# Optimization experiments

Measured on AMD Instinct MI355X. Metric: run time of the kernel, lower is better.

Reference implementation:

```python
import jax, jax.numpy as jnp
import numpy as np

EPS = 1e-6

def _rmsnorm(x, w):
    # fp32 RMSNorm over last dim
    var = jnp.mean(x * x, axis=-1, keepdims=True)
    return w * (x * jax.lax.rsqrt(var + EPS))

def setup_inputs() -> dict:
    key = jax.random.key(0)
    ks = jax.random.split(key, 6)
    S, D, H = 4096, 1024, 16
    HD = D // H
    return {
        "hidden_states": jax.random.normal(ks[0], (S, D), jnp.float32),
        "qkv_w": jax.random.normal(ks[1], (3 * D, D), jnp.float32) * 0.02,
        "qkv_b": jnp.zeros((3 * D,), jnp.float32),
        "proj_w": jax.random.normal(ks[2], (D, D), jnp.float32) * 0.02,
        "proj_b": jnp.zeros((D,), jnp.float32),
        "q_norm_w": jnp.ones((D,), jnp.float32),
        "k_norm_w": jnp.ones((D,), jnp.float32),
        "rotary_freqs": jax.random.normal(ks[3], (S, HD // 2), jnp.float32),
        "cu_seqlens": jnp.array([0, 1024, 2048, 3072, 4096], jnp.int32),
        "num_heads": 16,
    }

def reference(hidden_states, qkv_w, qkv_b, proj_w, proj_b, q_norm_w, k_norm_w, rotary_freqs, cu_seqlens, num_heads):
    S, D = hidden_states.shape
    H = num_heads
    hd = D // H
    # QKV projection
    qkv = hidden_states @ qkv_w.T + qkv_b           # [S, 3D]
    qkv = qkv.reshape(S, 3, H, hd)
    q, k, v = qkv[:, 0], qkv[:, 1], qkv[:, 2]       # each [S, H, hd]
    # QK RMSNorm over the flattened hidden dim (InternVL style)
    q = _rmsnorm(q.reshape(S, D), q_norm_w).reshape(S, H, hd)
    k = _rmsnorm(k.reshape(S, D), k_norm_w).reshape(S, H, hd)
    # RoPE: freqs [S, hd/2] -> cos/sin [S, 1, hd] (tiled, not interleaved)
    cos = jnp.cos(rotary_freqs)
    sin = jnp.sin(rotary_freqs)
    cos = jnp.concatenate([cos, cos], axis=-1)[:, None, :]
    sin = jnp.concatenate([sin, sin], axis=-1)[:, None, :]
    def rope(t):
        x1, x2 = jnp.split(t, 2, axis=-1)
        rot = jnp.concatenate([-x2, x1], axis=-1)
        return t * cos + rot * sin
    q = rope(q)
    k = rope(k)
    # Block-diagonal mask from cu_seqlens: same-segment tokens attend
    seg = jnp.searchsorted(cu_seqlens[1:], jnp.arange(S), side='right')  # [S]
    mask = seg[:, None] == seg[None, :]                                   # [S, S]
    scale = 1.0 / jnp.sqrt(jnp.float32(hd))
    scores = jnp.einsum('shd,thd->hst', q, k) * scale                     # [H, S, S]
    scores = jnp.where(mask[None], scores, jnp.float32(-1e30))
    probs = jax.nn.softmax(scores, axis=-1)
    out = jnp.einsum('hst,thd->shd', probs, v).reshape(S, D)
    return out @ proj_w.T + proj_b
```

## Files before the change

kernel.cpp:

```cpp
#include <hip/hip_runtime.h>
#include <hip/hip_bf16.h>

#define S 4096
#define D 1024
#define NH 16
#define HD 64

typedef float f32x4 __attribute__((ext_vector_type(4)));
typedef __bf16 bf16x8 __attribute__((ext_vector_type(8)));

#define MFMA16(a, b, c) __builtin_amdgcn_mfma_f32_16x16x32_bf16((a), (b), (c), 0, 0, 0)

__device__ __forceinline__ unsigned short f2bf(float f) {
  unsigned int u = __builtin_bit_cast(unsigned int, f);
  u += 0x7FFFu + ((u >> 16) & 1u);
  return (unsigned short)(u >> 16);
}

__device__ __forceinline__ float bf2f(unsigned short u) {
  unsigned int x = ((unsigned int)u) << 16;
  return __builtin_bit_cast(float, x);
}

__device__ __forceinline__ unsigned cvtpk(float lo, float hi) {
  unsigned r;
  asm("v_cvt_pk_bf16_f32 %0, %1, %2" : "=v"(r) : "v"(lo), "v"(hi));
  return r;
}

typedef __attribute__((address_space(1))) void GAS;
typedef __attribute__((address_space(3))) void LAS;

__device__ __forceinline__ void gld_lds16(const unsigned short* g, unsigned short* l) {
  __builtin_amdgcn_global_load_lds((GAS*)g, (LAS*)l, 16, 0, 0);
}

__global__ void cvt3(const float* __restrict__ a, unsigned short* __restrict__ ao,
                     const float* __restrict__ b, unsigned short* __restrict__ bo,
                     const float* __restrict__ c, unsigned short* __restrict__ co) {
  int i = blockIdx.x * blockDim.x + threadIdx.x;
  const float* in;
  unsigned short* out;
  int j;
  if (i < 1048576) { in = a; out = ao; j = i; }
  else if (i < 1835008) { in = b; out = bo; j = i - 1048576; }
  else { in = c; out = co; j = i - 1835008; }
  float4 v = ((const float4*)in)[j];
  ushort4 u;
  u.x = f2bf(v.x); u.y = f2bf(v.y); u.z = f2bf(v.z); u.w = f2bf(v.w);
  ((ushort4*)out)[j] = u;
}

__device__ __forceinline__ int xcd_swz(int bid, int nwg) {
  int q = nwg >> 3;
  return (bid & 7) * q + (bid >> 3);
}

#define DSTEP_S(RA, RB, SA, SB, KN, VM)                                          \
  {                                                                              \
    bf16x8 af[4], bfv[4];                                                        \
    _Pragma("unroll") for (int mf = 0; mf < 4; ++mf)                             \
        af[mf] = *(const bf16x8*)&RA[(wr * 64 + mf * 16 + l15) * 32 + l4 * 8];   \
    _Pragma("unroll") for (int nf = 0; nf < 4; ++nf)                             \
        bfv[nf] = *(const bf16x8*)&RB[(wc * 64 + nf * 16 + l15) * 32 + l4 * 8];  \
    gld_lds16(Ab + (size_t)r0 * 1024 + (KN) + o0, &SA[w * 512]);                 \
    gld_lds16(Ab + (size_t)r1 * 1024 + (KN) + o1, &SA[2048 + w * 512]);          \
    gld_lds16(Bb + (size_t)r0 * 1024 + (KN) + o0, &SB[w * 512]);                 \
    gld_lds16(Bb + (size_t)r1 * 1024 + (KN) + o1, &SB[2048 + w * 512]);          \
    _Pragma("unroll") for (int mf = 0; mf < 4; ++mf)                             \
        _Pragma("unroll") for (int nf = 0; nf < 4; ++nf)                         \
            acc[mf][nf] = MFMA16(af[mf], bfv[nf], acc[mf][nf]);                  \
    asm volatile("s_waitcnt vmcnt(" VM ")" ::: "memory");                        \
    __builtin_amdgcn_s_barrier();                                                \
  }

#define DSTEP_N(RA, RB, VM)                                                      \
  {                                                                              \
    bf16x8 af[4], bfv[4];                                                        \
    _Pragma("unroll") for (int mf = 0; mf < 4; ++mf)                             \
        af[mf] = *(const bf16x8*)&RA[(wr * 64 + mf * 16 + l15) * 32 + l4 * 8];   \
    _Pragma("unroll") for (int nf = 0; nf < 4; ++nf)                             \
        bfv[nf] = *(const bf16x8*)&RB[(wc * 64 + nf * 16 + l15) * 32 + l4 * 8];  \
    _Pragma("unroll") for (int mf = 0; mf < 4; ++mf)                             \
        _Pragma("unroll") for (int nf = 0; nf < 4; ++nf)                         \
            acc[mf][nf] = MFMA16(af[mf], bfv[nf], acc[mf][nf]);                  \
    asm volatile("s_waitcnt vmcnt(" VM ")" ::: "memory");                        \
    __builtin_amdgcn_s_barrier();                                                \
  }

#define DSTEP_LAST(RA, RB)                                                       \
  {                                                                              \
    bf16x8 af[4], bfv[4];                                                        \
    _Pragma("unroll") for (int mf = 0; mf < 4; ++mf)                             \
        af[mf] = *(const bf16x8*)&RA[(wr * 64 + mf * 16 + l15) * 32 + l4 * 8];   \
    _Pragma("unroll") for (int nf = 0; nf < 4; ++nf)                             \
        bfv[nf] = *(const bf16x8*)&RB[(wc * 64 + nf * 16 + l15) * 32 + l4 * 8];  \
    _Pragma("unroll") for (int mf = 0; mf < 4; ++mf)                             \
        _Pragma("unroll") for (int nf = 0; nf < 4; ++nf)                         \
            acc[mf][nf] = MFMA16(af[mf], bfv[nf], acc[mf][nf]);                  \
  }

#define GEMM_PRO_LOOP()                                                          \
  gld_lds16(Ab + (size_t)r0 * 1024 + o0, &As0[w * 512]);                         \
  gld_lds16(Ab + (size_t)r1 * 1024 + o1, &As0[2048 + w * 512]);                  \
  gld_lds16(Bb + (size_t)r0 * 1024 + o0, &Bs0[w * 512]);                         \
  gld_lds16(Bb + (size_t)r1 * 1024 + o1, &Bs0[2048 + w * 512]);                  \
  gld_lds16(Ab + (size_t)r0 * 1024 + 32 + o0, &As1[w * 512]);                    \
  gld_lds16(Ab + (size_t)r1 * 1024 + 32 + o1, &As1[2048 + w * 512]);             \
  gld_lds16(Bb + (size_t)r0 * 1024 + 32 + o0, &Bs1[w * 512]);                    \
  gld_lds16(Bb + (size_t)r1 * 1024 + 32 + o1, &Bs1[2048 + w * 512]);             \
  asm volatile("s_waitcnt vmcnt(4)" ::: "memory");                               \
  __builtin_amdgcn_s_barrier();                                                  \
  _Pragma("unroll 1") for (int k0 = 0; k0 < 960; k0 += 96) {                     \
    DSTEP_S(As0, Bs0, As2, Bs2, k0 + 64, "4")                                    \
    DSTEP_S(As1, Bs1, As0, Bs0, k0 + 96, "4")                                    \
    DSTEP_S(As2, Bs2, As1, Bs1, k0 + 128, "4")                                   \
  }                                                                              \
  DSTEP_N(As0, Bs0, "0")                                                         \
  DSTEP_LAST(As1, Bs1)

__global__ __launch_bounds__(256) void gemm_qkv(const unsigned short* __restrict__ A,
                                                const unsigned short* __restrict__ B,
                                                const float* __restrict__ bias,
                                                unsigned short* __restrict__ qk,
                                                unsigned short* __restrict__ vt) {
  __shared__ __align__(16) unsigned short As0[4096], As1[4096], As2[4096];
  __shared__ __align__(16) unsigned short Bs0[4096], Bs1[4096], Bs2[4096];
  __shared__ __align__(16) unsigned short tr[128 * 65];
  const int t = threadIdx.x;
  const int lane = t & 63;
  const int w = t >> 6;
  const int wr = w >> 1, wc = w & 1;
  const int l15 = lane & 15, l4 = lane >> 4;
  const int bid = blockIdx.y * 24 + blockIdx.x;
  const int r8 = bid & 7, i = bid >> 3;
  const int by = (r8 >> 1) * 8 + i / 12;
  const int bx = (r8 & 1) * 12 + i % 12;
  const int m0 = by * 128, n0 = bx * 128;

  f32x4 acc[4][4] = {};

  const int r0 = t >> 2, o0 = (t & 3) * 8;
  const int r1 = (256 + t) >> 2, o1 = ((256 + t) & 3) * 8;
  const unsigned short* Ab = A + (size_t)m0 * 1024;
  const unsigned short* Bb = B + (size_t)n0 * 1024;

  GEMM_PRO_LOOP()

  if (n0 < 2048) {
#pragma unroll
    for (int mf = 0; mf < 4; ++mf)
#pragma unroll
      for (int nf = 0; nf < 4; ++nf) {
        int rr = m0 + wr * 64 + mf * 16 + l4 * 4;
        int cc = n0 + wc * 64 + nf * 16 + l15;
        float bv = bias[cc];
#pragma unroll
        for (int j = 0; j < 4; ++j)
          qk[(size_t)(rr + j) * 2048 + cc] = f2bf(acc[mf][nf][j] + bv);
      }
  } else {
    const int h0 = (n0 - 2048) >> 6;
#pragma unroll
    for (int p = 0; p < 2; ++p) {
      __syncthreads();
      if (wc == p) {
#pragma unroll
        for (int mf = 0; mf < 4; ++mf)
#pragma unroll
          for (int nf = 0; nf < 4; ++nf) {
            int srow = wr * 64 + mf * 16 + l4 * 4;
            int cl = nf * 16 + l15;
            float bv = bias[n0 + p * 64 + cl];
#pragma unroll
            for (int j = 0; j < 4; ++j)
              tr[(srow + j) * 65 + cl] = f2bf(acc[mf][nf][j] + bv);
          }
      }
      __syncthreads();
      const int hh = h0 + p;
#pragma unroll
      for (int i2 = 0; i2 < 8; ++i2) {
        int idx = i2 * 256 + t;
        int d = idx >> 5, sc = idx & 31;
        ushort4 u;
        u.x = tr[(sc * 4 + 0) * 65 + d];
        u.y = tr[(sc * 4 + 1) * 65 + d];
        u.z = tr[(sc * 4 + 2) * 65 + d];
        u.w = tr[(sc * 4 + 3) * 65 + d];
        *(ushort4*)(vt + (size_t)hh * HD * S + (size_t)d * S + m0 + sc * 4) = u;
      }
    }
  }
}

__global__ __launch_bounds__(256) void gemm_bt(const unsigned short* __restrict__ A,
                                               const unsigned short* __restrict__ B,
                                               const float* __restrict__ bias,
                                               float* __restrict__ C,
                                               int M, int N, int K, int gx) {
  __shared__ __align__(16) unsigned short As0[4096], As1[4096], As2[4096];
  __shared__ __align__(16) unsigned short Bs0[4096], Bs1[4096], Bs2[4096];
  const int t = threadIdx.x;
  const int lane = t & 63;
  const int w = t >> 6;
  const int wr = w >> 1, wc = w & 1;
  const int l15 = lane & 15, l4 = lane >> 4;
  const int nwg = gridDim.x * gridDim.y;
  const int nbid = xcd_swz(blockIdx.y * gx + blockIdx.x, nwg);
  const int m0 = (nbid / gx) * 128, n0 = (nbid % gx) * 128;

  f32x4 acc[4][4] = {};

  const int r0 = t >> 2, o0 = (t & 3) * 8;
  const int r1 = (256 + t) >> 2, o1 = ((256 + t) & 3) * 8;
  const unsigned short* Ab = A + (size_t)m0 * 1024;
  const unsigned short* Bb = B + (size_t)n0 * 1024;

  GEMM_PRO_LOOP()

#pragma unroll
  for (int mf = 0; mf < 4; ++mf) {
#pragma unroll
    for (int nf = 0; nf < 4; ++nf) {
      int rr = m0 + wr * 64 + mf * 16 + l4 * 4;
      int cc = n0 + wc * 64 + nf * 16 + l15;
      float bv = bias[cc];
#pragma unroll
      for (int j = 0; j < 4; ++j)
        C[(size_t)(rr + j) * N + cc] = acc[mf][nf][j] + bv;
    }
  }
}

__global__ __launch_bounds__(256) void norm_rope(const unsigned short* __restrict__ qk,
                                                 const float* __restrict__ qw,
                                                 const float* __restrict__ kw,
                                                 const float* __restrict__ fr,
                                                 unsigned short* __restrict__ qo,
                                                 unsigned short* __restrict__ ko) {
  __shared__ float buf[1024];
  __shared__ float red[4];
  const int s = blockIdx.x, t = threadIdx.x;
  const int lane = t & 63, w = t >> 6;
  const int e = t * 4;
  const int hh = e >> 6, dd = e & 63;
  const float* frow = fr + (size_t)s * 32;
  float cs[4], sn[4];
#pragma unroll
  for (int i = 0; i < 4; ++i) {
    float f = frow[(dd + i) & 31];
    cs[i] = cosf(f);
    sn[i] = sinf(f);
  }
  for (int part = 0; part < 2; ++part) {
    const unsigned short* row = qk + (size_t)s * 2048 + part * 1024;
    const float* wvp = part ? kw : qw;
    unsigned short* op = part ? ko : qo;
    const float oscale = part ? 1.0f : 0.18033688011112042f;
    ushort4 uv = *(const ushort4*)(row + e);
    float vx = bf2f(uv.x), vy = bf2f(uv.y), vz = bf2f(uv.z), vw = bf2f(uv.w);
    float ssq = vx * vx + vy * vy + vz * vz + vw * vw;
#pragma unroll
    for (int off = 1; off < 64; off <<= 1) ssq += __shfl_xor(ssq, off, 64);
    if (part) __syncthreads();
    if (lane == 0) red[w] = ssq;
    __syncthreads();
    float inv = rsqrtf((red[0] + red[1] + red[2] + red[3]) * (1.0f / 1024.0f) + 1e-6f);
    float4 wv = *(const float4*)(wvp + e);
    buf[e + 0] = vx * inv * wv.x;
    buf[e + 1] = vy * inv * wv.y;
    buf[e + 2] = vz * inv * wv.z;
    buf[e + 3] = vw * inv * wv.w;
    __syncthreads();
    unsigned short ov[4];
#pragma unroll
    for (int i = 0; i < 4; ++i) {
      int di = dd + i;
      float x = buf[e + i];
      float rot = (di < 32) ? -buf[e + i + 32] : buf[e + i - 32];
      ov[i] = f2bf((x * cs[i] + rot * sn[i]) * oscale);
    }
    unsigned short* dst = op + (size_t)hh * S * HD + (size_t)s * HD + dd;
    dst[0] = ov[0]; dst[1] = ov[1]; dst[2] = ov[2]; dst[3] = ov[3];
  }
}

__device__ __forceinline__ void qk_tile(f32x4* s4, const unsigned short* Kbuf,
                                        bf16x8 qf0, bf16x8 qf1, int l15, int l4) {
#pragma unroll
  for (int nf = 0; nf < 4; ++nf) {
    const int row = nf * 16 + l15;
    const int roff = row * 64;
    const int sw = (row & 7) << 3;
    bf16x8 k0 = *(const bf16x8*)&Kbuf[roff + ((l4 * 8) ^ sw)];
    bf16x8 k1 = *(const bf16x8*)&Kbuf[roff + ((32 + l4 * 8) ^ sw)];
    s4[nf] = MFMA16(k0, qf0, s4[nf]);
    s4[nf] = MFMA16(k1, qf1, s4[nf]);
  }
}

__global__ __launch_bounds__(256) void attn_kernel(const unsigned short* __restrict__ q,
                                                   const unsigned short* __restrict__ k,
                                                   const unsigned short* __restrict__ vt,
                                                   unsigned short* __restrict__ aout) {
  __shared__ __align__(16) unsigned short Ks[2][4096];
  __shared__ __align__(16) unsigned short Vs[3][4096];
  const int bid = blockIdx.x;
  const int xcd = bid & 7;
  const int idx = bid >> 3;
  const int gw = idx >> 4, qt = idx & 15;
  const int g = xcd * 8 + gw;
  const int h = g >> 2, seg = g & 3;
  const int t = threadIdx.x, lane = t & 63, w = t >> 6;
  const int l15 = lane & 15, l4 = lane >> 4;
  const size_t hb = (size_t)h * S * HD;
  const int q0 = seg * 1024 + qt * 64 + w * 16;
  const int kvbase = seg * 1024;

  const int sr = t >> 3;
  const int scb = (t & 7) ^ (sr & 7);
  const unsigned short* ksrcA = k + hb + (size_t)(kvbase + sr) * HD + scb * 8;
  const unsigned short* ksrcB = ksrcA + 32 * HD;
  const unsigned short* vsrcA = vt + (size_t)h * HD * S + (size_t)sr * S + kvbase + scb * 8;
  const unsigned short* vsrcB = vsrcA + (size_t)32 * S;

  const unsigned short* qp = q + hb + (size_t)(q0 + l15) * HD + l4 * 8;
  bf16x8 qf0 = *(const bf16x8*)qp;
  bf16x8 qf1 = *(const bf16x8*)(qp + 32);

  f32x4 o[4] = {};
  float m = -1e30f, l = 0.f;

  gld_lds16(ksrcA, &Ks[0][w * 512]);
  gld_lds16(ksrcB, &Ks[0][2048 + w * 512]);
  gld_lds16(ksrcA + 4096, &Ks[1][w * 512]);
  gld_lds16(ksrcB + 4096, &Ks[1][2048 + w * 512]);
  gld_lds16(vsrcA, &Vs[0][w * 512]);
  gld_lds16(vsrcB, &Vs[0][2048 + w * 512]);
  gld_lds16(vsrcA + 64, &Vs[1][w * 512]);
  gld_lds16(vsrcB + 64, &Vs[1][2048 + w * 512]);
  __syncthreads();

  f32x4 cur[4] = {};
  qk_tile(cur, Ks[0], qf0, qf1, l15, l4);
  __syncthreads();

#pragma unroll
  for (int it = 0; it < 16; ++it) {
    if (it < 14) {
      gld_lds16(ksrcA + (it + 2) * 4096, &Ks[it & 1][w * 512]);
      gld_lds16(ksrcB + (it + 2) * 4096, &Ks[it & 1][2048 + w * 512]);
      gld_lds16(vsrcA + (it + 2) * 64, &Vs[(it + 2) % 3][w * 512]);
      gld_lds16(vsrcB + (it + 2) * 64, &Vs[(it + 2) % 3][2048 + w * 512]);
    }
    f32x4 nxt[4] = {};
    if (it < 15) {
      __builtin_amdgcn_s_setprio(1);
      qk_tile(nxt, Ks[(it + 1) & 1], qf0, qf1, l15, l4);
      __builtin_amdgcn_s_setprio(0);
      __builtin_amdgcn_sched_barrier(0);
    }
    float t0 = fmaxf(fmaxf(cur[0][0], cur[0][1]), cur[0][2]);
    float t1 = fmaxf(fmaxf(cur[0][3], cur[1][0]), cur[1][1]);
    float t2 = fmaxf(fmaxf(cur[1][2], cur[1][3]), cur[2][0]);
    float t3 = fmaxf(fmaxf(cur[2][1], cur[2][2]), cur[2][3]);
    float t4 = fmaxf(fmaxf(cur[3][0], cur[3][1]), cur[3][2]);
    float lmax = fmaxf(fmaxf(fmaxf(t0, t1), fmaxf(t2, t3)), fmaxf(t4, cur[3][3]));
    if (!__all(lmax <= m + 8.0f)) {
      float tmax = fmaxf(lmax, __shfl_xor(lmax, 16, 64));
      tmax = fmaxf(tmax, __shfl_xor(tmax, 32, 64));
      const float mn = fmaxf(m, tmax);
      const float corr = exp2f(m - mn);
      m = mn;
      l *= corr;
#pragma unroll
      for (int nf2 = 0; nf2 < 4; ++nf2)
#pragma unroll
        for (int j = 0; j < 4; ++j) o[nf2][j] *= corr;
    }
    float p[4][4];
#pragma unroll
    for (int nf = 0; nf < 4; ++nf)
#pragma unroll
      for (int j = 0; j < 4; ++j) {
        float e = exp2f(cur[nf][j] - m);
        p[nf][j] = e;
        l += e;
      }
    unsigned pk[4][2];
#pragma unroll
    for (int nf = 0; nf < 4; ++nf) {
      pk[nf][0] = cvtpk(p[nf][0], p[nf][1]);
      pk[nf][1] = cvtpk(p[nf][2], p[nf][3]);
    }
    const int srcbase = ((lane >> 4) & 1) * 32 + l15;
    const bool hi = (lane & 32) != 0;
    const unsigned short* Vbuf = Vs[it % 3];
#pragma unroll
    for (int ks = 0; ks < 2; ++ks) {
      unsigned bw[4];
#pragma unroll
      for (int h2 = 0; h2 < 2; ++h2)
#pragma unroll
        for (int r = 0; r < 2; ++r) {
          unsigned E = (unsigned)__shfl((int)pk[2 * ks][r], srcbase + h2 * 16, 64);
          unsigned F = (unsigned)__shfl((int)pk[2 * ks + 1][r], srcbase + h2 * 16, 64);
          bw[h2 * 2 + r] = hi ? F : E;
        }
      bf16x8 pb = __builtin_bit_cast(bf16x8, *(uint4*)bw);
      __builtin_amdgcn_s_setprio(1);
#pragma unroll
      for (int nf2 = 0; nf2 < 4; ++nf2) {
        const int row = nf2 * 16 + l15;
        const int roff = row * 64;
        const int sw = (row & 7) << 3;
        bf16x8 vf = *(const bf16x8*)&Vbuf[roff + ((ks * 32 + l4 * 8) ^ sw)];
        o[nf2] = MFMA16(vf, pb, o[nf2]);
      }
      __builtin_amdgcn_s_setprio(0);
    }
    __syncthreads();
    cur[0] = nxt[0]; cur[1] = nxt[1]; cur[2] = nxt[2]; cur[3] = nxt[3];
  }

  l += __shfl_xor(l, 16, 64);
  l += __shfl_xor(l, 32, 64);
  const float invl = 1.0f / l;
#pragma unroll
  for (int nf2 = 0; nf2 < 4; ++nf2) {
    ushort4 u;
    u.x = f2bf(o[nf2][0] * invl);
    u.y = f2bf(o[nf2][1] * invl);
    u.z = f2bf(o[nf2][2] * invl);
    u.w = f2bf(o[nf2][3] * invl);
    *(ushort4*)(aout + (size_t)(q0 + l15) * D + h * 64 + nf2 * 16 + l4 * 4) = u;
  }
}

extern "C" void kernel_launch(void* const* d_in, const int* in_sizes, int n_in,
                              void* d_out, int out_size, void* d_ws, size_t ws_size,
                              hipStream_t stream) {
  const float* hidden = (const float*)d_in[0];
  const float* qkvw   = (const float*)d_in[1];
  const float* qkvb   = (const float*)d_in[2];
  const float* projw  = (const float*)d_in[3];
  const float* projb  = (const float*)d_in[4];
  const float* qnw    = (const float*)d_in[5];
  const float* knw    = (const float*)d_in[6];
  const float* freqs  = (const float*)d_in[7];
  float* out = (float*)d_out;
  char* ws = (char*)d_ws;

  unsigned short* hb  = (unsigned short*)(ws + 0);
  unsigned short* wb  = (unsigned short*)(ws + (8u << 20));
  unsigned short* pb  = (unsigned short*)(ws + (14u << 20));
  unsigned short* qk  = (unsigned short*)(ws + (16u << 20));
  unsigned short* vtb = (unsigned short*)(ws + (32u << 20));
  unsigned short* qb  = (unsigned short*)(ws + (40u << 20));
  unsigned short* kb  = (unsigned short*)(ws + (48u << 20));
  unsigned short* ab  = (unsigned short*)(ws + (56u << 20));

  cvt3<<<8192, 256, 0, stream>>>(hidden, hb, qkvw, wb, projw, pb);
  gemm_qkv<<<dim3(24, 32), 256, 0, stream>>>(hb, wb, qkvb, qk, vtb);
  norm_rope<<<4096, 256, 0, stream>>>(qk, qnw, knw, freqs, qb, kb);
  attn_kernel<<<1024, 256, 0, stream>>>(qb, kb, vtb, ab);
  gemm_bt<<<dim3(8, 32), 256, 0, stream>>>(ab, pb, projb, out, 4096, 1024, 1024, 8);
}
```

Baseline: 126.4 us.

## Switch attention to 32x32x16 MFMA with 32 query rows per wave

Rewrites the attention inner loop to use the 32x32x16 bf16 MFMA instead of 16x16x32, so each wave handles 32 query rows and each block 128. This halves the grid and doubles the reuse of each K/V tile loaded into LDS. The P-matrix relayout now uses v_permlane32_swap instead of several ds_bpermute shuffles, and the row-max/row-sum reductions need fewer cross-lane steps. In exchange it uses more accumulator registers per wave and launches only 512 blocks, which may reduce occupancy and the ability to hide latency.

```diff
diff --git a/kernel.cpp b/kernel.cpp
--- a/kernel.cpp
+++ b/kernel.cpp
@@ -7,9 +7,11 @@
 #define HD 64
 
 typedef float f32x4 __attribute__((ext_vector_type(4)));
+typedef float f32x16 __attribute__((ext_vector_type(16)));
 typedef __bf16 bf16x8 __attribute__((ext_vector_type(8)));
 
 #define MFMA16(a, b, c) __builtin_amdgcn_mfma_f32_16x16x32_bf16((a), (b), (c), 0, 0, 0)
+#define MFMA32(a, b, c) __builtin_amdgcn_mfma_f32_32x32x16_bf16((a), (b), (c), 0, 0, 0)
 
 __device__ __forceinline__ unsigned short f2bf(float f) {
   unsigned int u = __builtin_bit_cast(unsigned int, f);
@@ -26,6 +28,17 @@
   unsigned r;
   asm("v_cvt_pk_bf16_f32 %0, %1, %2" : "=v"(r) : "v"(lo), "v"(hi));
   return r;
+}
+
+__device__ __forceinline__ void pl32swap(unsigned& a, unsigned& b) {
+#if __has_builtin(__builtin_amdgcn_permlane32_swap)
+  typedef unsigned u32x2 __attribute__((ext_vector_type(2)));
+  u32x2 r = __builtin_amdgcn_permlane32_swap(a, b, false, false);
+  a = r.x;
+  b = r.y;
+#else
+  asm volatile("v_permlane32_swap_b32 %0, %1" : "+v"(a), "+v"(b));
+#endif
 }
 
 typedef __attribute__((address_space(1))) void GAS;
@@ -286,17 +299,17 @@
   }
 }
 
-__device__ __forceinline__ void qk_tile(f32x4* s4, const unsigned short* Kbuf,
-                                        bf16x8 qf0, bf16x8 qf1, int l15, int l4) {
-#pragma unroll
-  for (int nf = 0; nf < 4; ++nf) {
-    const int row = nf * 16 + l15;
-    const int roff = row * 64;
-    const int sw = (row & 7) << 3;
-    bf16x8 k0 = *(const bf16x8*)&Kbuf[roff + ((l4 * 8) ^ sw)];
-    bf16x8 k1 = *(const bf16x8*)&Kbuf[roff + ((32 + l4 * 8) ^ sw)];
-    s4[nf] = MFMA16(k0, qf0, s4[nf]);
-    s4[nf] = MFMA16(k1, qf1, s4[nf]);
+__device__ __forceinline__ void qk_tile32(f32x16& s0, f32x16& s1,
+                                          const unsigned short* Kbuf,
+                                          const bf16x8* qB, int l31, int l5) {
+  const int x7 = l31 & 7;
+#pragma unroll
+  for (int c = 0; c < 4; ++c) {
+    const int ch = (2 * c + l5) ^ x7;
+    bf16x8 ka0 = *(const bf16x8*)&Kbuf[l31 * 64 + ch * 8];
+    bf16x8 ka1 = *(const bf16x8*)&Kbuf[(32 + l31) * 64 + ch * 8];
+    s0 = MFMA32(ka0, qB[c], s0);
+    s1 = MFMA32(ka1, qB[c], s1);
   }
 }
 
@@ -309,13 +322,13 @@
   const int bid = blockIdx.x;
   const int xcd = bid & 7;
   const int idx = bid >> 3;
-  const int gw = idx >> 4, qt = idx & 15;
+  const int gw = idx >> 3, qt = idx & 7;
   const int g = xcd * 8 + gw;
   const int h = g >> 2, seg = g & 3;
   const int t = threadIdx.x, lane = t & 63, w = t >> 6;
-  const int l15 = lane & 15, l4 = lane >> 4;
+  const int l31 = lane & 31, l5 = lane >> 5;
   const size_t hb = (size_t)h * S * HD;
-  const int q0 = seg * 1024 + qt * 64 + w * 16;
+  const int q0 = seg * 1024 + qt * 128 + w * 32;
   const int kvbase = seg * 1024;
 
   const int sr = t >> 3;
@@ -325,11 +338,12 @@
   const unsigned short* vsrcA = vt + (size_t)h * HD * S + (size_t)sr * S + kvbase + scb * 8;
   const unsigned short* vsrcB = vsrcA + (size_t)32 * S;
 
-  const unsigned short* qp = q + hb + (size_t)(q0 + l15) * HD + l4 * 8;
-  bf16x8 qf0 = *(const bf16x8*)qp;
-  bf16x8 qf1 = *(const bf16x8*)(qp + 32);
-
-  f32x4 o[4] = {};
+  const unsigned short* qp = q + hb + (size_t)(q0 + l31) * HD + l5 * 8;
+  bf16x8 qB[4];
+#pragma unroll
+  for (int c = 0; c < 4; ++c) qB[c] = *(const bf16x8*)(qp + 16 * c);
+
+  f32x16 o0 = {}, o1 = {};
   float m = -1e30f, l = 0.f;
 
   gld_lds16(ksrcA, &Ks[0][w * 512]);
@@ -342,8 +356,8 @@
   gld_lds16(vsrcB + 64, &Vs[1][2048 + w * 512]);
   __syncthreads();
 
-  f32x4 cur[4] = {};
-  qk_tile(cur, Ks[0], qf0, qf1, l15, l4);
+  f32x16 cur0 = {}, cur1 = {};
+  qk_tile32(cur0, cur1, Ks[0], qB, l31, l5);
   __syncthreads();
 
 #pragma unroll
@@ -354,87 +368,87 @@
       gld_lds16(vsrcA + (it + 2) * 64, &Vs[(it + 2) % 3][w * 512]);
       gld_lds16(vsrcB + (it + 2) * 64, &Vs[(it + 2) % 3][2048 + w * 512]);
     }
-    f32x4 nxt[4] = {};
+    f32x16 nxt0 = {}, nxt1 = {};
     if (it < 15) {
       __builtin_amdgcn_s_setprio(1);
-      qk_tile(nxt, Ks[(it + 1) & 1], qf0, qf1, l15, l4);
+      qk_tile32(nxt0, nxt1, Ks[(it + 1) & 1], qB, l31, l5);
       __builtin_amdgcn_s_setprio(0);
       __builtin_amdgcn_sched_barrier(0);
     }
-    float t0 = fmaxf(fmaxf(cur[0][0], cur[0][1]), cur[0][2]);
-    float t1 = fmaxf(fmaxf(cur[0][3], cur[1][0]), cur[1][1]);
-    float t2 = fmaxf(fmaxf(cur[1][2], cur[1][3]), cur[2][0]);
-    float t3 = fmaxf(fmaxf(cur[2][1], cur[2][2]), cur[2][3]);
-    float t4 = fmaxf(fmaxf(cur[3][0], cur[3][1]), cur[3][2]);
-    float lmax = fmaxf(fmaxf(fmaxf(t0, t1), fmaxf(t2, t3)), fmaxf(t4, cur[3][3]));
+    float mm[16];
+#pragma unroll
+    for (int i = 0; i < 16; ++i) mm[i] = fmaxf(cur0[i], cur1[i]);
+#pragma unroll
+    for (int st = 8; st > 0; st >>= 1)
+#pragma unroll
+      for (int i = 0; i < 8; ++i)
+        if (i < st) mm[i] = fmaxf(mm[i], mm[i + st]);
+    float lmax = fmaxf(mm[0], __shfl_xor(mm[0], 32, 64));
     if (!__all(lmax <= m + 8.0f)) {
-      float tmax = fmaxf(lmax, __shfl_xor(lmax, 16, 64));
-      tmax = fmaxf(tmax, __shfl_xor(tmax, 32, 64));
-      const float mn = fmaxf(m, tmax);
+      const float mn = fmaxf(m, lmax);
       const float corr = exp2f(m - mn);
       m = mn;
       l *= corr;
 #pragma unroll
-      for (int nf2 = 0; nf2 < 4; ++nf2)
-#pragma unroll
-        for (int j = 0; j < 4; ++j) o[nf2][j] *= corr;
-    }
-    float p[4][4];
-#pragma unroll
-    for (int nf = 0; nf < 4; ++nf)
-#pragma unroll
-      for (int j = 0; j < 4; ++j) {
-        float e = exp2f(cur[nf][j] - m);
-        p[nf][j] = e;
-        l += e;
-      }
-    unsigned pk[4][2];
-#pragma unroll
-    for (int nf = 0; nf < 4; ++nf) {
-      pk[nf][0] = cvtpk(p[nf][0], p[nf][1]);
-      pk[nf][1] = cvtpk(p[nf][2], p[nf][3]);
-    }
-    const int srcbase = ((lane >> 4) & 1) * 32 + l15;
-    const bool hi = (lane & 32) != 0;
+      for (int i = 0; i < 16; ++i) { o0[i] *= corr; o1[i] *= corr; }
+    }
+    unsigned pk0[8], pk1[8];
+    float ls0 = 0.f, ls1 = 0.f;
+#pragma unroll
+    for (int i = 0; i < 8; ++i) {
+      float a0 = exp2f(cur0[2 * i] - m), a1 = exp2f(cur0[2 * i + 1] - m);
+      float b0 = exp2f(cur1[2 * i] - m), b1 = exp2f(cur1[2 * i + 1] - m);
+      ls0 += a0 + a1;
+      ls1 += b0 + b1;
+      pk0[i] = cvtpk(a0, a1);
+      pk1[i] = cvtpk(b0, b1);
+    }
+    l += ls0 + ls1;
+    bf16x8 pB[4];
+#pragma unroll
+    for (int c = 0; c < 4; ++c) {
+      const int cl = c & 1;
+      unsigned w0, w1, w2, w3;
+      if (c < 2) { w0 = pk0[4 * cl + 0]; w1 = pk0[4 * cl + 1]; w2 = pk0[4 * cl + 2]; w3 = pk0[4 * cl + 3]; }
+      else       { w0 = pk1[4 * cl + 0]; w1 = pk1[4 * cl + 1]; w2 = pk1[4 * cl + 2]; w3 = pk1[4 * cl + 3]; }
+      pl32swap(w0, w2);
+      pl32swap(w1, w3);
+      uint4 bw;
+      bw.x = w0; bw.y = w1; bw.z = w2; bw.w = w3;
+      pB[c] = __builtin_bit_cast(bf16x8, bw);
+    }
     const unsigned short* Vbuf = Vs[it % 3];
-#pragma unroll
-    for (int ks = 0; ks < 2; ++ks) {
-      unsigned bw[4];
-#pragma unroll
-      for (int h2 = 0; h2 < 2; ++h2)
-#pragma unroll
-        for (int r = 0; r < 2; ++r) {
-          unsigned E = (unsigned)__shfl((int)pk[2 * ks][r], srcbase + h2 * 16, 64);
-          unsigned F = (unsigned)__shfl((int)pk[2 * ks + 1][r], srcbase + h2 * 16, 64);
-          bw[h2 * 2 + r] = hi ? F : E;
-        }
-      bf16x8 pb = __builtin_bit_cast(bf16x8, *(uint4*)bw);
-      __builtin_amdgcn_s_setprio(1);
-#pragma unroll
-      for (int nf2 = 0; nf2 < 4; ++nf2) {
-        const int row = nf2 * 16 + l15;
-        const int roff = row * 64;
-        const int sw = (row & 7) << 3;
-        bf16x8 vf = *(const bf16x8*)&Vbuf[roff + ((ks * 32 + l4 * 8) ^ sw)];
-        o[nf2] = MFMA16(vf, pb, o[nf2]);
-      }
-      __builtin_amdgcn_s_setprio(0);
-    }
+    const int x7 = l31 & 7;
+    __builtin_amdgcn_s_setprio(1);
+#pragma unroll
+    for (int c = 0; c < 4; ++c) {
+      const int ch = (2 * c + l5) ^ x7;
+      bf16x8 va0 = *(const bf16x8*)&Vbuf[l31 * 64 + ch * 8];
+      bf16x8 va1 = *(const bf16x8*)&Vbuf[(32 + l31) * 64 + ch * 8];
+      o0 = MFMA32(va0, pB[c], o0);
+      o1 = MFMA32(va1, pB[c], o1);
+    }
+    __builtin_amdgcn_s_setprio(0);
     __syncthreads();
-    cur[0] = nxt[0]; cur[1] = nxt[1]; cur[2] = nxt[2]; cur[3] = nxt[3];
-  }
-
-  l += __shfl_xor(l, 16, 64);
+    cur0 = nxt0;
+    cur1 = nxt1;
+  }
+
   l += __shfl_xor(l, 32, 64);
   const float invl = 1.0f / l;
 #pragma unroll
-  for (int nf2 = 0; nf2 < 4; ++nf2) {
-    ushort4 u;
-    u.x = f2bf(o[nf2][0] * invl);
-    u.y = f2bf(o[nf2][1] * invl);
-    u.z = f2bf(o[nf2][2] * invl);
-    u.w = f2bf(o[nf2][3] * invl);
-    *(ushort4*)(aout + (size_t)(q0 + l15) * D + h * 64 + nf2 * 16 + l4 * 4) = u;
+  for (int blk = 0; blk < 2; ++blk) {
+#pragma unroll
+    for (int rg = 0; rg < 4; ++rg) {
+      const f32x16& o = blk ? o1 : o0;
+      ushort4 u;
+      u.x = f2bf(o[4 * rg + 0] * invl);
+      u.y = f2bf(o[4 * rg + 1] * invl);
+      u.z = f2bf(o[4 * rg + 2] * invl);
+      u.w = f2bf(o[4 * rg + 3] * invl);
+      const int dcol = 32 * blk + 8 * rg + 4 * l5;
+      *(ushort4*)(aout + (size_t)(q0 + l31) * D + h * 64 + dcol) = u;
+    }
   }
 }
 
@@ -464,6 +478,6 @@
   cvt3<<<8192, 256, 0, stream>>>(hidden, hb, qkvw, wb, projw, pb);
   gemm_qkv<<<dim3(24, 32), 256, 0, stream>>>(hb, wb, qkvb, qk, vtb);
   norm_rope<<<4096, 256, 0, stream>>>(qk, qnw, knw, freqs, qb, kb);
-  attn_kernel<<<1024, 256, 0, stream>>>(qb, kb, vtb, ab);
+  attn_kernel<<<512, 256, 0, stream>>>(qb, kb, vtb, ab);
   gemm_bt<<<dim3(8, 32), 256, 0, stream>>>(ab, pb, projb, out, 4096, 1024, 1024, 8);
 }
```

Result: faster. 122.1 us (-3.4%).
